# Kernel optimization log

Hardware: AMD Instinct MI355X
Metric: run time of the kernel (lower is better)

Reference implementation:

```python
import jax, jax.numpy as jnp
import numpy as np

DIM = 512
NUM_HEADS = 8
B, NW, W = 8, 64, 64  # batch, num_windows, window_size


def setup_inputs() -> dict:
    key = jax.random.key(0)
    k1, k2, k3 = jax.random.split(key, 3)
    x = jax.random.normal(k1, (B, NW, W, DIM), dtype=jnp.float32)
    w_qkv = jax.random.normal(k2, (DIM, 3 * DIM), dtype=jnp.float32) * (DIM ** -0.5)
    w_proj = jax.random.normal(k3, (DIM, DIM), dtype=jnp.float32) * (DIM ** -0.5)
    b_proj = jnp.zeros((DIM,), dtype=jnp.float32)
    return {"x": x, "w_qkv": w_qkv, "w_proj": w_proj, "b_proj": b_proj}


def reference(x, w_qkv, w_proj, b_proj):
    batch, nw, w, dim = x.shape
    heads = NUM_HEADS
    dh = dim // heads
    scale = dh ** -0.5
    # qkv projection (no bias): [B, nW, W, 3*dim]
    qkv = jnp.einsum('bnwc,cd->bnwd', x, w_qkv)
    # -> [B, nW, W, 3, H, dh] -> [3, B, H, nW, W, dh]
    qkv = qkv.reshape(batch, nw, w, 3, heads, dh)
    qkv = jnp.transpose(qkv, (3, 0, 4, 1, 2, 5))
    q, k, v = qkv[0], qkv[1], qkv[2]
    # attention logits per window: [B, H, nW, W, W]
    attn = jnp.einsum('bhnqd,bhnkd->bhnqk', q, k) * scale
    attn = jax.nn.softmax(attn, axis=-1)
    # [B, H, nW, W, dh]
    out = jnp.einsum('bhnqk,bhnkd->bhnqd', attn, v)
    # faithful raw reshape (no transpose), matching the TF source
    out = out.reshape(batch, nw, w, dim)
    return jnp.einsum('bnwc,cd->bnwd', out, w_proj) + b_proj
```

## Files before the change

kernel.cpp:

```cpp
#include <hip/hip_runtime.h>
#include <hip/hip_bf16.h>

typedef __bf16 bf16_t;
typedef __bf16 bf16x8 __attribute__((ext_vector_type(8)));
typedef float f32x4 __attribute__((ext_vector_type(4)));
typedef float f32x16 __attribute__((ext_vector_type(16)));

#define GLOAD_LDS16(gp, lp) __builtin_amdgcn_global_load_lds( \
    (const __attribute__((address_space(1))) void*)(gp),      \
    (__attribute__((address_space(3))) void*)(lp), 16, 0, 0)

__device__ __forceinline__ int swz64(int row, int col) {
    return row * 64 + (col ^ ((row & 7) << 3));
}

__global__ __launch_bounds__(256) void transpose_cast_kernel(
    const float* __restrict__ src, bf16_t* __restrict__ dst, int R, int C)
{
    __shared__ float tile[32][33];
    const int bx = blockIdx.x;
    const int by = blockIdx.y;
    const int t  = threadIdx.x;
    const int i0 = t >> 5;
    const int j  = t & 31;
#pragma unroll
    for (int p = 0; p < 4; ++p) {
        int i = i0 + p * 8;
        tile[i][j] = src[(long)(by * 32 + i) * C + bx * 32 + j];
    }
    __syncthreads();
#pragma unroll
    for (int p = 0; p < 4; ++p) {
        int i = i0 + p * 8;
        dst[(long)(bx * 32 + i) * R + by * 32 + j] = (bf16_t)tile[j][i];
    }
}

__global__ __launch_bounds__(256) void cast_x_kernel(
    const float* __restrict__ src, bf16_t* __restrict__ dst, long n8)
{
    long i = (long)blockIdx.x * blockDim.x + threadIdx.x;
    const long stride = (long)gridDim.x * blockDim.x;
    for (; i < n8; i += stride) {
        const float* p = src + i * 8;
        f32x4 f0 = *(const f32x4*)p;
        f32x4 f1 = *(const f32x4*)(p + 4);
        bf16x8 o;
        o[0] = (bf16_t)f0[0]; o[1] = (bf16_t)f0[1];
        o[2] = (bf16_t)f0[2]; o[3] = (bf16_t)f0[3];
        o[4] = (bf16_t)f1[0]; o[5] = (bf16_t)f1[1];
        o[6] = (bf16_t)f1[2]; o[7] = (bf16_t)f1[3];
        *(bf16x8*)(dst + i * 8) = o;
    }
}

__global__ __launch_bounds__(256, 2) void qkv_attn_kernel(
    const bf16_t* __restrict__ xb,
    const bf16_t* __restrict__ wT,
    bf16_t* __restrict__ ao)
{
    __shared__ bf16_t arena[40960];
    bf16_t* const buf0 = arena;
    bf16_t* const buf1 = arena + 20480;

    const int id   = blockIdx.x;
    const int xcd  = id & 7;
    const int s    = id >> 3;
    const int pr   = xcd * 32 + (s >> 3);
    const int h    = s & 7;
    const int wid0 = pr * 2;

    const bf16_t* xw = xb + (long)wid0 * 64 * 512;

    const int t    = threadIdx.x;
    const int wv   = t >> 6;
    const int lane = t & 63;
    const int wm   = wv >> 1;
    const int wn   = wv & 1;
    const int l31  = lane & 31;
    const int l5   = lane >> 5;
    const int rlo  = lane >> 3;
    const int ch   = (lane & 7) ^ rlo;

    bf16_t* const lQw = arena +     0 + wm * 12288;
    bf16_t* const lKw = arena +  4096 + wm * 12288;
    bf16_t* const lVw = arena +  8192 + wm * 12288;
    bf16_t* const lPw = arena + 24576 + wm * 4096;

    auto stage = [&](bf16_t* buf, int k0) {
#pragma unroll
        for (int p = 0; p < 4; ++p) {
            const int rb = wv * 4 + p;
            GLOAD_LDS16(xw + (long)(rb * 8 + rlo) * 512 + k0 + ch * 8,
                        buf + rb * 512);
        }
#pragma unroll
        for (int j = 0; j < 6; ++j) {
            const int rb = wv * 6 + j;
            const int nr = rb * 8 + rlo;
            const int grow = ((nr >> 6) << 9) + h * 64 + (nr & 63);
            GLOAD_LDS16(wT + (long)grow * 512 + k0 + ch * 8,
                        buf + 8192 + rb * 512);
        }
    };

    f32x16 acc[2][3];
#pragma unroll
    for (int mi = 0; mi < 2; ++mi)
#pragma unroll
        for (int ni = 0; ni < 3; ++ni) acc[mi][ni] = (f32x16)0.0f;

    auto compute = [&](const bf16_t* lX, const bf16_t* lW) {
#pragma unroll
        for (int ks = 0; ks < 64; ks += 16) {
            bf16x8 a0 = *(const bf16x8*)&lX[swz64(wm * 64 +  0 + l31, ks + l5 * 8)];
            bf16x8 a1 = *(const bf16x8*)&lX[swz64(wm * 64 + 32 + l31, ks + l5 * 8)];
#pragma unroll
            for (int ni = 0; ni < 3; ++ni) {
                bf16x8 b = *(const bf16x8*)&lW[swz64(wn * 96 + ni * 32 + l31, ks + l5 * 8)];
                acc[0][ni] = __builtin_amdgcn_mfma_f32_32x32x16_bf16(a0, b, acc[0][ni], 0, 0, 0);
                acc[1][ni] = __builtin_amdgcn_mfma_f32_32x32x16_bf16(a1, b, acc[1][ni], 0, 0, 0);
            }
        }
    };

    stage(buf0, 0);
    __syncthreads();
#pragma unroll 1
    for (int kc2 = 0; kc2 < 4; ++kc2) {
        const int kc = kc2 * 2;
        stage(buf1, (kc + 1) * 64);
        compute(buf0, buf0 + 8192);
        __syncthreads();
        if (kc + 2 < 8) stage(buf0, (kc + 2) * 64);
        compute(buf1, buf1 + 8192);
        __syncthreads();
    }

#pragma unroll
    for (int mi = 0; mi < 2; ++mi) {
#pragma unroll
        for (int ni = 0; ni < 3; ++ni) {
            const int n = wn * 96 + ni * 32 + l31;
            const int g = n >> 6;
            const int c = n & 63;
#pragma unroll
            for (int r = 0; r < 16; ++r) {
                const int tk = mi * 32 + (r & 3) + ((r >> 2) << 3) + (l5 << 2);
                const bf16_t val = (bf16_t)acc[mi][ni][r];
                if (g == 0)      lQw[swz64(tk, c)] = val;
                else if (g == 1) lKw[swz64(tk, c)] = val;
                else             lVw[swz64(c, tk)] = val;
            }
        }
    }
    __syncthreads();

    const int lr = lane & 15;
    const int q  = lane >> 4;
    const int qh = wn * 32;
    const float scale = 0.125f;

    f32x4 sA[2][4];
#pragma unroll
    for (int i = 0; i < 2; ++i)
#pragma unroll
        for (int j = 0; j < 4; ++j) sA[i][j] = (f32x4)0.0f;
#pragma unroll
    for (int ks = 0; ks < 64; ks += 32) {
        bf16x8 aq0 = *(const bf16x8*)&lQw[swz64(qh +  0 + lr, ks + q * 8)];
        bf16x8 aq1 = *(const bf16x8*)&lQw[swz64(qh + 16 + lr, ks + q * 8)];
#pragma unroll
        for (int j = 0; j < 4; ++j) {
            bf16x8 bk = *(const bf16x8*)&lKw[swz64(j * 16 + lr, ks + q * 8)];
            sA[0][j] = __builtin_amdgcn_mfma_f32_16x16x32_bf16(aq0, bk, sA[0][j], 0, 0, 0);
            sA[1][j] = __builtin_amdgcn_mfma_f32_16x16x32_bf16(aq1, bk, sA[1][j], 0, 0, 0);
        }
    }

#pragma unroll
    for (int i = 0; i < 2; ++i)
#pragma unroll
    for (int reg = 0; reg < 4; ++reg) {
        float m = fmaxf(fmaxf(sA[i][0][reg], sA[i][1][reg]),
                        fmaxf(sA[i][2][reg], sA[i][3][reg]));
#pragma unroll
        for (int d = 1; d < 16; d <<= 1) m = fmaxf(m, __shfl_xor(m, d));
        float p[4];
        float sum = 0.0f;
#pragma unroll
        for (int j = 0; j < 4; ++j) {
            p[j] = __expf((sA[i][j][reg] - m) * scale);
            sum += p[j];
        }
#pragma unroll
        for (int d = 1; d < 16; d <<= 1) sum += __shfl_xor(sum, d);
        const float inv = 1.0f / sum;
        const int row = qh + i * 16 + q * 4 + reg;
#pragma unroll
        for (int j = 0; j < 4; ++j)
            lPw[swz64(row, j * 16 + lr)] = (bf16_t)(p[j] * inv);
    }

    f32x4 o[2][4];
#pragma unroll
    for (int i = 0; i < 2; ++i)
#pragma unroll
        for (int d4 = 0; d4 < 4; ++d4) o[i][d4] = (f32x4)0.0f;
#pragma unroll
    for (int ks = 0; ks < 64; ks += 32) {
        bf16x8 ap0 = *(const bf16x8*)&lPw[swz64(qh +  0 + lr, ks + q * 8)];
        bf16x8 ap1 = *(const bf16x8*)&lPw[swz64(qh + 16 + lr, ks + q * 8)];
#pragma unroll
        for (int d4 = 0; d4 < 4; ++d4) {
            bf16x8 bv = *(const bf16x8*)&lVw[swz64(d4 * 16 + lr, ks + q * 8)];
            o[0][d4] = __builtin_amdgcn_mfma_f32_16x16x32_bf16(ap0, bv, o[0][d4], 0, 0, 0);
            o[1][d4] = __builtin_amdgcn_mfma_f32_16x16x32_bf16(ap1, bv, o[1][d4], 0, 0, 0);
        }
    }

    const int wid = wid0 + wm;
    const int bb  = wid >> 6;
    const int nw  = wid & 63;
    bf16_t* aop = ao + ((long)bb * 4096 + (long)h * 512 + nw * 8) * 512;
#pragma unroll
    for (int i = 0; i < 2; ++i)
#pragma unroll
    for (int d4 = 0; d4 < 4; ++d4)
#pragma unroll
    for (int reg = 0; reg < 4; ++reg) {
        const int wr = qh + i * 16 + q * 4 + reg;
        aop[(long)(wr >> 3) * 512 + (wr & 7) * 64 + d4 * 16 + lr] =
            (bf16_t)o[i][d4][reg];
    }
}

__global__ __launch_bounds__(256) void gemm2_kernel(
    const bf16_t* __restrict__ A,
    const bf16_t* __restrict__ Bt,
    const float*  __restrict__ bias,
    float* __restrict__ C,
    int M, int N, int K)
{
    __shared__ bf16_t lA[8192];
    __shared__ bf16_t lB[8192];

    const int tid  = threadIdx.x;
    const int wave = tid >> 6;
    const int lane = tid & 63;
    const int wm   = wave >> 1;
    const int wn   = wave & 1;
    const int lr   = lane & 15;
    const int q    = lane >> 4;
    const int rlo  = lane >> 3;
    const int ch   = (lane & 7) ^ rlo;

    const int id  = blockIdx.x;
    const int xcd = id & 7;
    const int s   = id >> 3;
    const int bm  = xcd * 32 + (s >> 2);
    const int bn  = s & 3;

    const long arow0 = (long)bm * 128;
    const long brow0 = (long)bn * 128;

    f32x4 acc[4][4];
#pragma unroll
    for (int i = 0; i < 4; ++i)
#pragma unroll
        for (int j = 0; j < 4; ++j) acc[i][j] = (f32x4)0.0f;

    const int nk = K / 64;
    for (int kt = 0; kt < nk; ++kt) {
        const long k0 = kt * 64;
#pragma unroll
        for (int p = 0; p < 4; ++p) {
            const int rb = wave * 4 + p;
            const int r  = rb * 8 + rlo;
            GLOAD_LDS16(A  + (arow0 + r) * (long)K + k0 + ch * 8, lA + rb * 512);
            GLOAD_LDS16(Bt + (brow0 + r) * (long)K + k0 + ch * 8, lB + rb * 512);
        }
        __syncthreads();
#pragma unroll
        for (int ks = 0; ks < 64; ks += 32) {
            bf16x8 af[4], bf[4];
#pragma unroll
            for (int i = 0; i < 4; ++i)
                af[i] = *(const bf16x8*)&lA[swz64(wm * 64 + i * 16 + lr, ks + q * 8)];
#pragma unroll
            for (int j = 0; j < 4; ++j)
                bf[j] = *(const bf16x8*)&lB[swz64(wn * 64 + j * 16 + lr, ks + q * 8)];
#pragma unroll
            for (int i = 0; i < 4; ++i)
#pragma unroll
                for (int j = 0; j < 4; ++j)
                    acc[i][j] = __builtin_amdgcn_mfma_f32_16x16x32_bf16(
                        af[i], bf[j], acc[i][j], 0, 0, 0);
        }
        __syncthreads();
    }

#pragma unroll
    for (int i = 0; i < 4; ++i) {
        const long r = arow0 + wm * 64 + i * 16 + q * 4;
#pragma unroll
        for (int j = 0; j < 4; ++j) {
            const long c = brow0 + wn * 64 + j * 16 + lr;
            const float bv2 = bias[c];
#pragma unroll
            for (int reg = 0; reg < 4; ++reg) {
                C[(r + reg) * N + c] = acc[i][j][reg] + bv2;
            }
        }
    }
}

extern "C" void kernel_launch(void* const* d_in, const int* in_sizes, int n_in,
                              void* d_out, int out_size, void* d_ws, size_t ws_size,
                              hipStream_t stream)
{
    (void)in_sizes; (void)n_in; (void)out_size;
    const float* x     = (const float*)d_in[0];
    const float* wqkv  = (const float*)d_in[1];
    const float* wproj = (const float*)d_in[2];
    const float* bproj = (const float*)d_in[3];
    float* out = (float*)d_out;

    bf16_t* wT = (bf16_t*)d_ws;
    bf16_t* pT = wT + (size_t)1536 * 512;
    bf16_t* ao = pT + (size_t)512 * 512;

    const size_t base_elems = (size_t)1536 * 512 + (size_t)512 * 512
                            + (size_t)32768 * 512;
    const size_t xb_elems   = (size_t)32768 * 512;
    bf16_t* xb = (ws_size >= (base_elems + xb_elems) * sizeof(bf16_t))
               ? (ao + xb_elems)
               : (bf16_t*)d_out;

    transpose_cast_kernel<<<dim3(48, 16), 256, 0, stream>>>(wqkv, wT, 512, 1536);
    transpose_cast_kernel<<<dim3(16, 16), 256, 0, stream>>>(wproj, pT, 512, 512);
    cast_x_kernel<<<2048, 256, 0, stream>>>(x, xb, (long)32768 * 512 / 8);

    qkv_attn_kernel<<<2048, 256, 0, stream>>>(xb, wT, ao);

    gemm2_kernel<<<1024, 256, 0, stream>>>(
        ao, pT, bproj, out, 32768, 512, 512);
}
```

Baseline: 228.7 us.

## Fuse x fp32-to-bf16 cast into QKV kernel, load A directly to registers

Removes the separate cast_x kernel and its bf16 copy of x. The QKV+attention kernel now reads fp32 x straight from global memory into registers, converts it to bf16 MFMA A-fragments there, and stages only the weight tiles through LDS. With the smaller LDS arena it raises launch bounds to 3 blocks per CU and aliases the P buffer onto Q. The V transpose store is also vectorised to 4-wide bf16 writes. In exchange, each of the 8 heads sharing a window pair re-reads fp32 x (twice the bytes of bf16) without LDS staging or prefetch, so A loads are exposed latency inside the k-loop.

```diff
diff --git a/kernel.cpp b/kernel.cpp
--- a/kernel.cpp
+++ b/kernel.cpp
@@ -2,6 +2,7 @@
 #include <hip/hip_bf16.h>
 
 typedef __bf16 bf16_t;
+typedef __bf16 bf16x4 __attribute__((ext_vector_type(4)));
 typedef __bf16 bf16x8 __attribute__((ext_vector_type(8)));
 typedef float f32x4 __attribute__((ext_vector_type(4)));
 typedef float f32x16 __attribute__((ext_vector_type(16)));
@@ -36,32 +37,14 @@
     }
 }
 
-__global__ __launch_bounds__(256) void cast_x_kernel(
-    const float* __restrict__ src, bf16_t* __restrict__ dst, long n8)
-{
-    long i = (long)blockIdx.x * blockDim.x + threadIdx.x;
-    const long stride = (long)gridDim.x * blockDim.x;
-    for (; i < n8; i += stride) {
-        const float* p = src + i * 8;
-        f32x4 f0 = *(const f32x4*)p;
-        f32x4 f1 = *(const f32x4*)(p + 4);
-        bf16x8 o;
-        o[0] = (bf16_t)f0[0]; o[1] = (bf16_t)f0[1];
-        o[2] = (bf16_t)f0[2]; o[3] = (bf16_t)f0[3];
-        o[4] = (bf16_t)f1[0]; o[5] = (bf16_t)f1[1];
-        o[6] = (bf16_t)f1[2]; o[7] = (bf16_t)f1[3];
-        *(bf16x8*)(dst + i * 8) = o;
-    }
-}
-
-__global__ __launch_bounds__(256, 2) void qkv_attn_kernel(
-    const bf16_t* __restrict__ xb,
+__global__ __launch_bounds__(256, 3) void qkv_attn_kernel(
+    const float*  __restrict__ x,
     const bf16_t* __restrict__ wT,
     bf16_t* __restrict__ ao)
 {
-    __shared__ bf16_t arena[40960];
-    bf16_t* const buf0 = arena;
-    bf16_t* const buf1 = arena + 20480;
+    __shared__ bf16_t arena[24576];
+    bf16_t* const wbuf0 = arena;
+    bf16_t* const wbuf1 = arena + 12288;
 
     const int id   = blockIdx.x;
     const int xcd  = id & 7;
@@ -70,7 +53,7 @@
     const int h    = s & 7;
     const int wid0 = pr * 2;
 
-    const bf16_t* xw = xb + (long)wid0 * 64 * 512;
+    const float* xw = x + (long)wid0 * 64 * 512;
 
     const int t    = threadIdx.x;
     const int wv   = t >> 6;
@@ -82,25 +65,19 @@
     const int rlo  = lane >> 3;
     const int ch   = (lane & 7) ^ rlo;
 
-    bf16_t* const lQw = arena +     0 + wm * 12288;
-    bf16_t* const lKw = arena +  4096 + wm * 12288;
-    bf16_t* const lVw = arena +  8192 + wm * 12288;
-    bf16_t* const lPw = arena + 24576 + wm * 4096;
-
-    auto stage = [&](bf16_t* buf, int k0) {
-#pragma unroll
-        for (int p = 0; p < 4; ++p) {
-            const int rb = wv * 4 + p;
-            GLOAD_LDS16(xw + (long)(rb * 8 + rlo) * 512 + k0 + ch * 8,
-                        buf + rb * 512);
-        }
+    bf16_t* const lQw = arena +    0 + wm * 12288;
+    bf16_t* const lKw = arena + 4096 + wm * 12288;
+    bf16_t* const lVw = arena + 8192 + wm * 12288;
+    bf16_t* const lPw = lQw;
+
+    auto stageW = [&](bf16_t* buf, int k0) {
 #pragma unroll
         for (int j = 0; j < 6; ++j) {
             const int rb = wv * 6 + j;
             const int nr = rb * 8 + rlo;
             const int grow = ((nr >> 6) << 9) + h * 64 + (nr & 63);
             GLOAD_LDS16(wT + (long)grow * 512 + k0 + ch * 8,
-                        buf + 8192 + rb * 512);
+                        buf + rb * 512);
         }
     };
 
@@ -110,30 +87,48 @@
 #pragma unroll
         for (int ni = 0; ni < 3; ++ni) acc[mi][ni] = (f32x16)0.0f;
 
-    auto compute = [&](const bf16_t* lX, const bf16_t* lW) {
-#pragma unroll
-        for (int ks = 0; ks < 64; ks += 16) {
-            bf16x8 a0 = *(const bf16x8*)&lX[swz64(wm * 64 +  0 + l31, ks + l5 * 8)];
-            bf16x8 a1 = *(const bf16x8*)&lX[swz64(wm * 64 + 32 + l31, ks + l5 * 8)];
+    auto computeW = [&](const bf16_t* lW, int k0) {
+        bf16x8 aw[8];
+#pragma unroll
+        for (int ksi = 0; ksi < 4; ++ksi)
+#pragma unroll
+            for (int mi2 = 0; mi2 < 2; ++mi2) {
+                const float* p = xw + (long)(wm * 64 + mi2 * 32 + l31) * 512
+                               + k0 + ksi * 16 + l5 * 8;
+                f32x4 f0 = *(const f32x4*)p;
+                f32x4 f1 = *(const f32x4*)(p + 4);
+                bf16x8 o;
+                o[0] = (bf16_t)f0[0]; o[1] = (bf16_t)f0[1];
+                o[2] = (bf16_t)f0[2]; o[3] = (bf16_t)f0[3];
+                o[4] = (bf16_t)f1[0]; o[5] = (bf16_t)f1[1];
+                o[6] = (bf16_t)f1[2]; o[7] = (bf16_t)f1[3];
+                aw[ksi * 2 + mi2] = o;
+            }
+#pragma unroll
+        for (int ksi = 0; ksi < 4; ++ksi) {
+            const int ks = ksi * 16;
 #pragma unroll
             for (int ni = 0; ni < 3; ++ni) {
-                bf16x8 b = *(const bf16x8*)&lW[swz64(wn * 96 + ni * 32 + l31, ks + l5 * 8)];
-                acc[0][ni] = __builtin_amdgcn_mfma_f32_32x32x16_bf16(a0, b, acc[0][ni], 0, 0, 0);
-                acc[1][ni] = __builtin_amdgcn_mfma_f32_32x32x16_bf16(a1, b, acc[1][ni], 0, 0, 0);
+                bf16x8 b = *(const bf16x8*)&lW[swz64(wn * 96 + ni * 32 + l31,
+                                                    ks + l5 * 8)];
+                acc[0][ni] = __builtin_amdgcn_mfma_f32_32x32x16_bf16(
+                    aw[ksi * 2 + 0], b, acc[0][ni], 0, 0, 0);
+                acc[1][ni] = __builtin_amdgcn_mfma_f32_32x32x16_bf16(
+                    aw[ksi * 2 + 1], b, acc[1][ni], 0, 0, 0);
             }
         }
     };
 
-    stage(buf0, 0);
+    stageW(wbuf0, 0);
     __syncthreads();
 #pragma unroll 1
     for (int kc2 = 0; kc2 < 4; ++kc2) {
         const int kc = kc2 * 2;
-        stage(buf1, (kc + 1) * 64);
-        compute(buf0, buf0 + 8192);
+        stageW(wbuf1, (kc + 1) * 64);
+        computeW(wbuf0, kc * 64);
         __syncthreads();
-        if (kc + 2 < 8) stage(buf0, (kc + 2) * 64);
-        compute(buf1, buf1 + 8192);
+        if (kc + 2 < 8) stageW(wbuf0, (kc + 2) * 64);
+        computeW(wbuf1, (kc + 1) * 64);
         __syncthreads();
     }
 
@@ -144,13 +139,25 @@
             const int n = wn * 96 + ni * 32 + l31;
             const int g = n >> 6;
             const int c = n & 63;
-#pragma unroll
-            for (int r = 0; r < 16; ++r) {
-                const int tk = mi * 32 + (r & 3) + ((r >> 2) << 3) + (l5 << 2);
-                const bf16_t val = (bf16_t)acc[mi][ni][r];
-                if (g == 0)      lQw[swz64(tk, c)] = val;
-                else if (g == 1) lKw[swz64(tk, c)] = val;
-                else             lVw[swz64(c, tk)] = val;
+            if (g == 2) {
+#pragma unroll
+                for (int rq = 0; rq < 4; ++rq) {
+                    const int tk0 = mi * 32 + 8 * rq + 4 * l5;
+                    bf16x4 pk;
+                    pk[0] = (bf16_t)acc[mi][ni][rq * 4 + 0];
+                    pk[1] = (bf16_t)acc[mi][ni][rq * 4 + 1];
+                    pk[2] = (bf16_t)acc[mi][ni][rq * 4 + 2];
+                    pk[3] = (bf16_t)acc[mi][ni][rq * 4 + 3];
+                    *(bf16x4*)&lVw[swz64(c, tk0)] = pk;
+                }
+            } else {
+#pragma unroll
+                for (int r = 0; r < 16; ++r) {
+                    const int tk = mi * 32 + (r & 3) + ((r >> 2) << 3) + (l5 << 2);
+                    const bf16_t val = (bf16_t)acc[mi][ni][r];
+                    if (g == 0) lQw[swz64(tk, c)] = val;
+                    else        lKw[swz64(tk, c)] = val;
+                }
             }
         }
     }
@@ -319,7 +326,7 @@
                               void* d_out, int out_size, void* d_ws, size_t ws_size,
                               hipStream_t stream)
 {
-    (void)in_sizes; (void)n_in; (void)out_size;
+    (void)in_sizes; (void)n_in; (void)out_size; (void)ws_size;
     const float* x     = (const float*)d_in[0];
     const float* wqkv  = (const float*)d_in[1];
     const float* wproj = (const float*)d_in[2];
@@ -330,18 +337,10 @@
     bf16_t* pT = wT + (size_t)1536 * 512;
     bf16_t* ao = pT + (size_t)512 * 512;
 
-    const size_t base_elems = (size_t)1536 * 512 + (size_t)512 * 512
-                            + (size_t)32768 * 512;
-    const size_t xb_elems   = (size_t)32768 * 512;
-    bf16_t* xb = (ws_size >= (base_elems + xb_elems) * sizeof(bf16_t))
-               ? (ao + xb_elems)
-               : (bf16_t*)d_out;
-
     transpose_cast_kernel<<<dim3(48, 16), 256, 0, stream>>>(wqkv, wT, 512, 1536);
     transpose_cast_kernel<<<dim3(16, 16), 256, 0, stream>>>(wproj, pT, 512, 512);
-    cast_x_kernel<<<2048, 256, 0, stream>>>(x, xb, (long)32768 * 512 / 8);
-
-    qkv_attn_kernel<<<2048, 256, 0, stream>>>(xb, wT, ao);
+
+    qkv_attn_kernel<<<2048, 256, 0, stream>>>(x, wT, ao);
 
     gemm2_kernel<<<1024, 256, 0, stream>>>(
         ao, pT, bproj, out, 32768, 512, 512);
```

After: 291.7 us. 1.28x slower.

## Restructure fused QKV-attention kernel to 8 waves with register-held x operands

Applied to the files above, without the earlier changes.

The fused QKV+attention kernel now uses 512 threads (8 waves), each owning a 32-row slice of x, and loads its x MFMA operands straight from global memory into registers. Only the weight tile is staged in LDS, which shrinks the LDS arena from 80KB to 48KB. The attention phase gives each wave 16 query rows of one window and reuses the Q region for P. V is written to LDS with packed 4-wide stores. The goal is higher occupancy and less LDS traffic, at the cost of uncoalesced direct global x loads and higher register pressure per wave.

```diff
diff --git a/kernel.cpp b/kernel.cpp
--- a/kernel.cpp
+++ b/kernel.cpp
@@ -2,6 +2,7 @@
 #include <hip/hip_bf16.h>
 
 typedef __bf16 bf16_t;
+typedef __bf16 bf16x4 __attribute__((ext_vector_type(4)));
 typedef __bf16 bf16x8 __attribute__((ext_vector_type(8)));
 typedef float f32x4 __attribute__((ext_vector_type(4)));
 typedef float f32x16 __attribute__((ext_vector_type(16)));
@@ -54,14 +55,14 @@
     }
 }
 
-__global__ __launch_bounds__(256, 2) void qkv_attn_kernel(
+__global__ __launch_bounds__(512, 4) void qkv_attn_kernel(
     const bf16_t* __restrict__ xb,
     const bf16_t* __restrict__ wT,
     bf16_t* __restrict__ ao)
 {
-    __shared__ bf16_t arena[40960];
-    bf16_t* const buf0 = arena;
-    bf16_t* const buf1 = arena + 20480;
+    __shared__ bf16_t arena[24576];
+    bf16_t* const wbuf0 = arena;
+    bf16_t* const wbuf1 = arena + 12288;
 
     const int id   = blockIdx.x;
     const int xcd  = id & 7;
@@ -75,163 +76,168 @@
     const int t    = threadIdx.x;
     const int wv   = t >> 6;
     const int lane = t & 63;
-    const int wm   = wv >> 1;
-    const int wn   = wv & 1;
+    const int wr   = wv >> 1;
+    const int wc   = wv & 1;
     const int l31  = lane & 31;
     const int l5   = lane >> 5;
     const int rlo  = lane >> 3;
     const int ch   = (lane & 7) ^ rlo;
 
-    bf16_t* const lQw = arena +     0 + wm * 12288;
-    bf16_t* const lKw = arena +  4096 + wm * 12288;
-    bf16_t* const lVw = arena +  8192 + wm * 12288;
-    bf16_t* const lPw = arena + 24576 + wm * 4096;
-
-    auto stage = [&](bf16_t* buf, int k0) {
-#pragma unroll
-        for (int p = 0; p < 4; ++p) {
-            const int rb = wv * 4 + p;
-            GLOAD_LDS16(xw + (long)(rb * 8 + rlo) * 512 + k0 + ch * 8,
-                        buf + rb * 512);
-        }
-#pragma unroll
-        for (int j = 0; j < 6; ++j) {
-            const int rb = wv * 6 + j;
+    auto stageW = [&](bf16_t* buf, int k0) {
+#pragma unroll
+        for (int j = 0; j < 3; ++j) {
+            const int rb = wv * 3 + j;
             const int nr = rb * 8 + rlo;
             const int grow = ((nr >> 6) << 9) + h * 64 + (nr & 63);
-            GLOAD_LDS16(wT + (long)grow * 512 + k0 + ch * 8,
-                        buf + 8192 + rb * 512);
+            GLOAD_LDS16(wT + (long)grow * 512 + k0 + ch * 8, buf + rb * 512);
         }
     };
-
-    f32x16 acc[2][3];
-#pragma unroll
-    for (int mi = 0; mi < 2; ++mi)
-#pragma unroll
-        for (int ni = 0; ni < 3; ++ni) acc[mi][ni] = (f32x16)0.0f;
-
-    auto compute = [&](const bf16_t* lX, const bf16_t* lW) {
-#pragma unroll
-        for (int ks = 0; ks < 64; ks += 16) {
-            bf16x8 a0 = *(const bf16x8*)&lX[swz64(wm * 64 +  0 + l31, ks + l5 * 8)];
-            bf16x8 a1 = *(const bf16x8*)&lX[swz64(wm * 64 + 32 + l31, ks + l5 * 8)];
+    auto loadx = [&](bf16x8* a, int k0) {
+        const bf16_t* rp = xw + (long)(wr * 32 + l31) * 512 + k0 + l5 * 8;
+#pragma unroll
+        for (int ksi = 0; ksi < 4; ++ksi)
+            a[ksi] = *(const bf16x8*)(rp + ksi * 16);
+    };
+
+    f32x16 acc[3];
+#pragma unroll
+    for (int ni = 0; ni < 3; ++ni) acc[ni] = (f32x16)0.0f;
+
+    auto compute = [&](const bf16x8* a, const bf16_t* lW) {
+#pragma unroll
+        for (int ksi = 0; ksi < 4; ++ksi) {
+            const int ks = ksi * 16;
 #pragma unroll
             for (int ni = 0; ni < 3; ++ni) {
-                bf16x8 b = *(const bf16x8*)&lW[swz64(wn * 96 + ni * 32 + l31, ks + l5 * 8)];
-                acc[0][ni] = __builtin_amdgcn_mfma_f32_32x32x16_bf16(a0, b, acc[0][ni], 0, 0, 0);
-                acc[1][ni] = __builtin_amdgcn_mfma_f32_32x32x16_bf16(a1, b, acc[1][ni], 0, 0, 0);
+                bf16x8 b = *(const bf16x8*)&lW[swz64(wc * 96 + ni * 32 + l31,
+                                                    ks + l5 * 8)];
+                acc[ni] = __builtin_amdgcn_mfma_f32_32x32x16_bf16(
+                    a[ksi], b, acc[ni], 0, 0, 0);
             }
         }
     };
 
-    stage(buf0, 0);
+    bf16x8 aC[4], aN[4];
+    stageW(wbuf0, 0);
+    loadx(aC, 0);
     __syncthreads();
 #pragma unroll 1
     for (int kc2 = 0; kc2 < 4; ++kc2) {
         const int kc = kc2 * 2;
-        stage(buf1, (kc + 1) * 64);
-        compute(buf0, buf0 + 8192);
+        stageW(wbuf1, (kc + 1) * 64);
+        loadx(aN, (kc + 1) * 64);
+        compute(aC, wbuf0);
         __syncthreads();
-        if (kc + 2 < 8) stage(buf0, (kc + 2) * 64);
-        compute(buf1, buf1 + 8192);
+        if (kc2 < 3) {
+            stageW(wbuf0, (kc + 2) * 64);
+            loadx(aC, (kc + 2) * 64);
+        }
+        compute(aN, wbuf1);
         __syncthreads();
     }
 
-#pragma unroll
-    for (int mi = 0; mi < 2; ++mi) {
-#pragma unroll
-        for (int ni = 0; ni < 3; ++ni) {
-            const int n = wn * 96 + ni * 32 + l31;
-            const int g = n >> 6;
-            const int c = n & 63;
+    const int swin = wr >> 1;
+    bf16_t* const sQ = arena + swin * 12288;
+    bf16_t* const sK = sQ + 4096;
+    bf16_t* const sV = sQ + 8192;
+#pragma unroll
+    for (int ni = 0; ni < 3; ++ni) {
+        const int n = wc * 96 + ni * 32 + l31;
+        const int g = n >> 6;
+        const int c = n & 63;
+        if (g == 2) {
+#pragma unroll
+            for (int rq = 0; rq < 4; ++rq) {
+                const int tl0 = (wr & 1) * 32 + 8 * rq + 4 * l5;
+                bf16x4 pk;
+                pk[0] = (bf16_t)acc[ni][rq * 4 + 0];
+                pk[1] = (bf16_t)acc[ni][rq * 4 + 1];
+                pk[2] = (bf16_t)acc[ni][rq * 4 + 2];
+                pk[3] = (bf16_t)acc[ni][rq * 4 + 3];
+                *(bf16x4*)&sV[swz64(c, tl0)] = pk;
+            }
+        } else {
 #pragma unroll
             for (int r = 0; r < 16; ++r) {
-                const int tk = mi * 32 + (r & 3) + ((r >> 2) << 3) + (l5 << 2);
-                const bf16_t val = (bf16_t)acc[mi][ni][r];
-                if (g == 0)      lQw[swz64(tk, c)] = val;
-                else if (g == 1) lKw[swz64(tk, c)] = val;
-                else             lVw[swz64(c, tk)] = val;
+                const int tl = (wr & 1) * 32 + (r & 3) + ((r >> 2) << 3) + (l5 << 2);
+                const bf16_t val = (bf16_t)acc[ni][r];
+                if (g == 0) sQ[swz64(tl, c)] = val;
+                else        sK[swz64(tl, c)] = val;
             }
         }
     }
     __syncthreads();
+
+    const int win = wv >> 2;
+    const int qb  = wv & 3;
+    bf16_t* const lQ = arena + win * 12288;
+    bf16_t* const lK = lQ + 4096;
+    bf16_t* const lV = lQ + 8192;
+    bf16_t* const lP = lQ;
 
     const int lr = lane & 15;
     const int q  = lane >> 4;
-    const int qh = wn * 32;
     const float scale = 0.125f;
 
-    f32x4 sA[2][4];
-#pragma unroll
-    for (int i = 0; i < 2; ++i)
-#pragma unroll
-        for (int j = 0; j < 4; ++j) sA[i][j] = (f32x4)0.0f;
+    f32x4 sA[4];
+#pragma unroll
+    for (int j = 0; j < 4; ++j) sA[j] = (f32x4)0.0f;
 #pragma unroll
     for (int ks = 0; ks < 64; ks += 32) {
-        bf16x8 aq0 = *(const bf16x8*)&lQw[swz64(qh +  0 + lr, ks + q * 8)];
-        bf16x8 aq1 = *(const bf16x8*)&lQw[swz64(qh + 16 + lr, ks + q * 8)];
+        bf16x8 aq = *(const bf16x8*)&lQ[swz64(qb * 16 + lr, ks + q * 8)];
 #pragma unroll
         for (int j = 0; j < 4; ++j) {
-            bf16x8 bk = *(const bf16x8*)&lKw[swz64(j * 16 + lr, ks + q * 8)];
-            sA[0][j] = __builtin_amdgcn_mfma_f32_16x16x32_bf16(aq0, bk, sA[0][j], 0, 0, 0);
-            sA[1][j] = __builtin_amdgcn_mfma_f32_16x16x32_bf16(aq1, bk, sA[1][j], 0, 0, 0);
-        }
-    }
-
-#pragma unroll
-    for (int i = 0; i < 2; ++i)
+            bf16x8 bk = *(const bf16x8*)&lK[swz64(j * 16 + lr, ks + q * 8)];
+            sA[j] = __builtin_amdgcn_mfma_f32_16x16x32_bf16(aq, bk, sA[j], 0, 0, 0);
+        }
+    }
+
 #pragma unroll
     for (int reg = 0; reg < 4; ++reg) {
-        float m = fmaxf(fmaxf(sA[i][0][reg], sA[i][1][reg]),
-                        fmaxf(sA[i][2][reg], sA[i][3][reg]));
+        float m = fmaxf(fmaxf(sA[0][reg], sA[1][reg]),
+                        fmaxf(sA[2][reg], sA[3][reg]));
 #pragma unroll
         for (int d = 1; d < 16; d <<= 1) m = fmaxf(m, __shfl_xor(m, d));
         float p[4];
         float sum = 0.0f;
 #pragma unroll
         for (int j = 0; j < 4; ++j) {
-            p[j] = __expf((sA[i][j][reg] - m) * scale);
+            p[j] = __expf((sA[j][reg] - m) * scale);
             sum += p[j];
         }
 #pragma unroll
         for (int d = 1; d < 16; d <<= 1) sum += __shfl_xor(sum, d);
         const float inv = 1.0f / sum;
-        const int row = qh + i * 16 + q * 4 + reg;
+        const int row = qb * 16 + q * 4 + reg;
 #pragma unroll
         for (int j = 0; j < 4; ++j)
-            lPw[swz64(row, j * 16 + lr)] = (bf16_t)(p[j] * inv);
-    }
-
-    f32x4 o[2][4];
-#pragma unroll
-    for (int i = 0; i < 2; ++i)
-#pragma unroll
-        for (int d4 = 0; d4 < 4; ++d4) o[i][d4] = (f32x4)0.0f;
+            lP[swz64(row, j * 16 + lr)] = (bf16_t)(p[j] * inv);
+    }
+
+    f32x4 o[4];
+#pragma unroll
+    for (int d4 = 0; d4 < 4; ++d4) o[d4] = (f32x4)0.0f;
 #pragma unroll
     for (int ks = 0; ks < 64; ks += 32) {
-        bf16x8 ap0 = *(const bf16x8*)&lPw[swz64(qh +  0 + lr, ks + q * 8)];
-        bf16x8 ap1 = *(const bf16x8*)&lPw[swz64(qh + 16 + lr, ks + q * 8)];
+        bf16x8 ap = *(const bf16x8*)&lP[swz64(qb * 16 + lr, ks + q * 8)];
 #pragma unroll
         for (int d4 = 0; d4 < 4; ++d4) {
-            bf16x8 bv = *(const bf16x8*)&lVw[swz64(d4 * 16 + lr, ks + q * 8)];
-            o[0][d4] = __builtin_amdgcn_mfma_f32_16x16x32_bf16(ap0, bv, o[0][d4], 0, 0, 0);
-            o[1][d4] = __builtin_amdgcn_mfma_f32_16x16x32_bf16(ap1, bv, o[1][d4], 0, 0, 0);
-        }
-    }
-
-    const int wid = wid0 + wm;
+            bf16x8 bv = *(const bf16x8*)&lV[swz64(d4 * 16 + lr, ks + q * 8)];
+            o[d4] = __builtin_amdgcn_mfma_f32_16x16x32_bf16(ap, bv, o[d4], 0, 0, 0);
+        }
+    }
+
+    const int wid = wid0 + win;
     const int bb  = wid >> 6;
     const int nw  = wid & 63;
     bf16_t* aop = ao + ((long)bb * 4096 + (long)h * 512 + nw * 8) * 512;
 #pragma unroll
-    for (int i = 0; i < 2; ++i)
-#pragma unroll
     for (int d4 = 0; d4 < 4; ++d4)
 #pragma unroll
     for (int reg = 0; reg < 4; ++reg) {
-        const int wr = qh + i * 16 + q * 4 + reg;
-        aop[(long)(wr >> 3) * 512 + (wr & 7) * 64 + d4 * 16 + lr] =
-            (bf16_t)o[i][d4][reg];
+        const int tok = qb * 16 + q * 4 + reg;
+        aop[(long)(tok >> 3) * 512 + (tok & 7) * 64 + d4 * 16 + lr] =
+            (bf16_t)o[d4][reg];
     }
 }
 
@@ -341,7 +347,7 @@
     transpose_cast_kernel<<<dim3(16, 16), 256, 0, stream>>>(wproj, pT, 512, 512);
     cast_x_kernel<<<2048, 256, 0, stream>>>(x, xb, (long)32768 * 512 / 8);
 
-    qkv_attn_kernel<<<2048, 256, 0, stream>>>(xb, wT, ao);
+    qkv_attn_kernel<<<2048, 512, 0, stream>>>(xb, wT, ao);
 
     gemm2_kernel<<<1024, 256, 0, stream>>>(
         ao, pT, bproj, out, 32768, 512, 512);
```

After: 243.0 us. 6.3% more time.

## Double-buffer gemm2 with vmcnt waits, relax qkv pipeline barriers, vectorize V stores

Applied to the files above, without the earlier changes.

The output projection GEMM moves from a single LDS buffer to ping-pong buffers. The next K-tile is issued with global_load_lds before computing the current one, and partial s_waitcnt vmcnt replaces the full __syncthreads drains. The fused qkv/attention kernel gets the same treatment: explicit vmcnt, sched_barrier and s_barrier, plus s_setprio around the MFMA loops. The transposed V tile is now written to LDS as packed 4-wide bf16 stores instead of scalar stores. This doubles gemm2's LDS footprint and makes correctness depend on hand-counted outstanding loads per wave, where a wrong count could introduce a race.

```diff
diff --git a/kernel.cpp b/kernel.cpp
--- a/kernel.cpp
+++ b/kernel.cpp
@@ -2,6 +2,7 @@
 #include <hip/hip_bf16.h>
 
 typedef __bf16 bf16_t;
+typedef __bf16 bf16x4 __attribute__((ext_vector_type(4)));
 typedef __bf16 bf16x8 __attribute__((ext_vector_type(8)));
 typedef float f32x4 __attribute__((ext_vector_type(4)));
 typedef float f32x16 __attribute__((ext_vector_type(16)));
@@ -9,6 +10,10 @@
 #define GLOAD_LDS16(gp, lp) __builtin_amdgcn_global_load_lds( \
     (const __attribute__((address_space(1))) void*)(gp),      \
     (__attribute__((address_space(3))) void*)(lp), 16, 0, 0)
+
+#define VMCNT(n) asm volatile("s_waitcnt vmcnt(" #n ")" ::: "memory")
+#define SCHED_FENCE() __builtin_amdgcn_sched_barrier(0)
+#define BARRIER() __builtin_amdgcn_s_barrier()
 
 __device__ __forceinline__ int swz64(int row, int col) {
     return row * 64 + (col ^ ((row & 7) << 3));
@@ -111,6 +116,7 @@
         for (int ni = 0; ni < 3; ++ni) acc[mi][ni] = (f32x16)0.0f;
 
     auto compute = [&](const bf16_t* lX, const bf16_t* lW) {
+        __builtin_amdgcn_s_setprio(1);
 #pragma unroll
         for (int ks = 0; ks < 64; ks += 16) {
             bf16x8 a0 = *(const bf16x8*)&lX[swz64(wm * 64 +  0 + l31, ks + l5 * 8)];
@@ -122,19 +128,31 @@
                 acc[1][ni] = __builtin_amdgcn_mfma_f32_32x32x16_bf16(a1, b, acc[1][ni], 0, 0, 0);
             }
         }
+        __builtin_amdgcn_s_setprio(0);
     };
 
     stage(buf0, 0);
-    __syncthreads();
 #pragma unroll 1
     for (int kc2 = 0; kc2 < 4; ++kc2) {
         const int kc = kc2 * 2;
         stage(buf1, (kc + 1) * 64);
+        VMCNT(10);
+        SCHED_FENCE();
+        BARRIER();
         compute(buf0, buf0 + 8192);
-        __syncthreads();
-        if (kc + 2 < 8) stage(buf0, (kc + 2) * 64);
+        SCHED_FENCE();
+        BARRIER();
+        if (kc2 < 3) {
+            stage(buf0, (kc + 2) * 64);
+            VMCNT(10);
+        } else {
+            VMCNT(0);
+        }
+        SCHED_FENCE();
+        BARRIER();
         compute(buf1, buf1 + 8192);
-        __syncthreads();
+        SCHED_FENCE();
+        BARRIER();
     }
 
 #pragma unroll
@@ -144,13 +162,25 @@
             const int n = wn * 96 + ni * 32 + l31;
             const int g = n >> 6;
             const int c = n & 63;
-#pragma unroll
-            for (int r = 0; r < 16; ++r) {
-                const int tk = mi * 32 + (r & 3) + ((r >> 2) << 3) + (l5 << 2);
-                const bf16_t val = (bf16_t)acc[mi][ni][r];
-                if (g == 0)      lQw[swz64(tk, c)] = val;
-                else if (g == 1) lKw[swz64(tk, c)] = val;
-                else             lVw[swz64(c, tk)] = val;
+            if (g == 2) {
+#pragma unroll
+                for (int rq = 0; rq < 4; ++rq) {
+                    const int tk0 = mi * 32 + 8 * rq + 4 * l5;
+                    bf16x4 pk;
+                    pk[0] = (bf16_t)acc[mi][ni][rq * 4 + 0];
+                    pk[1] = (bf16_t)acc[mi][ni][rq * 4 + 1];
+                    pk[2] = (bf16_t)acc[mi][ni][rq * 4 + 2];
+                    pk[3] = (bf16_t)acc[mi][ni][rq * 4 + 3];
+                    *(bf16x4*)&lVw[swz64(c, tk0)] = pk;
+                }
+            } else {
+#pragma unroll
+                for (int r = 0; r < 16; ++r) {
+                    const int tk = mi * 32 + (r & 3) + ((r >> 2) << 3) + (l5 << 2);
+                    const bf16_t val = (bf16_t)acc[mi][ni][r];
+                    if (g == 0) lQw[swz64(tk, c)] = val;
+                    else        lKw[swz64(tk, c)] = val;
+                }
             }
         }
     }
@@ -242,8 +272,11 @@
     float* __restrict__ C,
     int M, int N, int K)
 {
-    __shared__ bf16_t lA[8192];
-    __shared__ bf16_t lB[8192];
+    __shared__ bf16_t arena[32768];
+    bf16_t* const lA0 = arena;
+    bf16_t* const lB0 = arena + 8192;
+    bf16_t* const lA1 = arena + 16384;
+    bf16_t* const lB1 = arena + 24576;
 
     const int tid  = threadIdx.x;
     const int wave = tid >> 6;
@@ -270,17 +303,18 @@
 #pragma unroll
         for (int j = 0; j < 4; ++j) acc[i][j] = (f32x4)0.0f;
 
-    const int nk = K / 64;
-    for (int kt = 0; kt < nk; ++kt) {
-        const long k0 = kt * 64;
+    auto stage = [&](bf16_t* bA, bf16_t* bB, long k0) {
 #pragma unroll
         for (int p = 0; p < 4; ++p) {
             const int rb = wave * 4 + p;
             const int r  = rb * 8 + rlo;
-            GLOAD_LDS16(A  + (arow0 + r) * (long)K + k0 + ch * 8, lA + rb * 512);
-            GLOAD_LDS16(Bt + (brow0 + r) * (long)K + k0 + ch * 8, lB + rb * 512);
-        }
-        __syncthreads();
+            GLOAD_LDS16(A  + (arow0 + r) * (long)K + k0 + ch * 8, bA + rb * 512);
+            GLOAD_LDS16(Bt + (brow0 + r) * (long)K + k0 + ch * 8, bB + rb * 512);
+        }
+    };
+
+    auto compute = [&](const bf16_t* lA, const bf16_t* lB) {
+        __builtin_amdgcn_s_setprio(1);
 #pragma unroll
         for (int ks = 0; ks < 64; ks += 32) {
             bf16x8 af[4], bf[4];
@@ -297,7 +331,31 @@
                     acc[i][j] = __builtin_amdgcn_mfma_f32_16x16x32_bf16(
                         af[i], bf[j], acc[i][j], 0, 0, 0);
         }
-        __syncthreads();
+        __builtin_amdgcn_s_setprio(0);
+    };
+
+    stage(lA0, lB0, 0);
+#pragma unroll 1
+    for (int kt2 = 0; kt2 < 4; ++kt2) {
+        const int kt = kt2 * 2;
+        stage(lA1, lB1, (long)(kt + 1) * 64);
+        VMCNT(8);
+        SCHED_FENCE();
+        BARRIER();
+        compute(lA0, lB0);
+        SCHED_FENCE();
+        BARRIER();
+        if (kt2 < 3) {
+            stage(lA0, lB0, (long)(kt + 2) * 64);
+            VMCNT(8);
+        } else {
+            VMCNT(0);
+        }
+        SCHED_FENCE();
+        BARRIER();
+        compute(lA1, lB1);
+        SCHED_FENCE();
+        BARRIER();
     }
 
 #pragma unroll
```

New measurement: 209.8 us. 1.09x faster.
